# Performance work log

Measured on AMD Instinct MI355X. Metric: run time of the kernel, lower is better.

## Reference

```python
import jax, jax.numpy as jnp
import numpy as np

K = 32
BN_EPS = 1e-5


def setup_inputs() -> dict:
    key = jax.random.key(0)
    ks = jax.random.split(key, 4)
    B, Cin, N, C = 8, 1152, 4096, 128
    return {
        "x": jax.random.normal(ks[0], (B, Cin, N), dtype=jnp.float32),
        "W1": jax.random.normal(ks[1], (C, Cin), dtype=jnp.float32) * 0.02,
        "bn_gamma": jnp.ones((C,), jnp.float32),
        "bn_beta": jnp.zeros((C,), jnp.float32),
        "bn_mean": jnp.zeros((C,), jnp.float32),
        "bn_var": jnp.ones((C,), jnp.float32),
        "Wq": jax.random.normal(ks[2], (C, C), dtype=jnp.float32) * 0.05,
        "Wk": jax.random.normal(ks[3], (C, C), dtype=jnp.float32) * 0.05,
    }


def _forward(x, W1, bn_gamma, bn_beta, bn_mean, bn_var, Wq, Wk):
    # conv1: 1x1 Conv1d (no bias) + BatchNorm (inference stats) + LeakyReLU(0.2)
    h = jnp.einsum('oc,bcn->bon', W1, x)                       # [B,128,N]
    h = (h - bn_mean[None, :, None]) * jax.lax.rsqrt(bn_var + BN_EPS)[None, :, None]
    h = h * bn_gamma[None, :, None] + bn_beta[None, :, None]
    h = jnp.where(h >= 0, h, 0.2 * h)
    f = jnp.transpose(h, (0, 2, 1))                            # [B,N,128]

    # ops.group: feature-space KNN + 'diff' grouping
    sq = jnp.sum(f * f, axis=-1)                               # [B,N]
    dist = sq[:, :, None] + sq[:, None, :] - 2.0 * jnp.einsum('bnc,bmc->bnm', f, f)
    _, idx = jax.lax.top_k(-dist, K)                           # [B,N,K]
    nb = jax.vmap(lambda fb, ib: fb[ib])(f, idx)               # [B,N,K,128]
    diff = nb - f[:, :, None, :]                               # neighbors - center

    # q/k 1x1 convs, per-point 1xK attention
    q = jnp.einsum('bnc,oc->bno', f, Wq)                       # [B,N,128]
    k = jnp.einsum('bnkc,oc->bnko', diff, Wk)                  # [B,N,K,128]
    energy = jnp.einsum('bnc,bnkc->bnk', q, k) / jnp.sqrt(jnp.float32(q.shape[-1]))
    attn = jax.nn.softmax(energy, axis=-1)                     # [B,N,K]

    # std over K (biased), then per-cloud standardize (unbiased std, torch default)
    s = jnp.std(attn, axis=-1)                                 # [B,N]
    mean = jnp.mean(s, axis=1, keepdims=True)
    std = jnp.std(s, axis=1, keepdims=True, ddof=1)
    z = (s - mean) / std
    return 1.0 / (1.0 + jnp.power(jnp.float32(20.0), -z))      # modified sigmoid


def reference(x, W1, bn_gamma, bn_beta, bn_mean, bn_var, Wq, Wk):
    return _forward(x, W1, bn_gamma, bn_beta, bn_mean, bn_var, Wq, Wk)
```

## Files before the change

### kernel.cpp

```cpp
#include <hip/hip_runtime.h>
#include <math.h>

#define B_   8
#define CIN  1152
#define NPTS 4096
#define CH   128
#define KNN  32

__global__ __launch_bounds__(256) void k_conv_bn(
    const float* __restrict__ x, const float* __restrict__ W1,
    const float* __restrict__ gamma, const float* __restrict__ beta,
    const float* __restrict__ bmean, const float* __restrict__ bvar,
    float* __restrict__ f)
{
  __shared__ float Wl[8][132];
  __shared__ float Xl[8][64];
  int bid = blockIdx.x;
  int b = bid & 7;
  int nbase = (bid >> 3) * 64;
  int t = threadIdx.x;
  int c0 = (t & 31) * 4, n0 = (t >> 5) * 8;
  double acc[4][8];
#pragma unroll
  for (int i = 0; i < 4; ++i)
#pragma unroll
    for (int j = 0; j < 8; ++j) acc[i][j] = 0.0;

  for (int k0 = 0; k0 < CIN; k0 += 8) {
    {
      int c = t >> 1, kp = (t & 1) * 4;
      float4 w4 = *(const float4*)&W1[(size_t)c * CIN + k0 + kp];
      Wl[kp + 0][c] = w4.x; Wl[kp + 1][c] = w4.y;
      Wl[kp + 2][c] = w4.z; Wl[kp + 3][c] = w4.w;
    }
    {
      int k = t >> 5, n = (t & 31) * 2;
      float2 x2 = *(const float2*)&x[((size_t)b * CIN + (k0 + k)) * NPTS + nbase + n];
      Xl[k][n] = x2.x; Xl[k][n + 1] = x2.y;
    }
    __syncthreads();
#pragma unroll
    for (int kk = 0; kk < 8; ++kk) {
      float4 a  = *(const float4*)&Wl[kk][c0];
      float4 b0 = *(const float4*)&Xl[kk][n0];
      float4 b1 = *(const float4*)&Xl[kk][n0 + 4];
      double av[4] = {(double)a.x, (double)a.y, (double)a.z, (double)a.w};
      double bv[8] = {(double)b0.x, (double)b0.y, (double)b0.z, (double)b0.w,
                      (double)b1.x, (double)b1.y, (double)b1.z, (double)b1.w};
#pragma unroll
      for (int i = 0; i < 4; ++i)
#pragma unroll
        for (int j = 0; j < 8; ++j) acc[i][j] = fma(av[i], bv[j], acc[i][j]);
    }
    __syncthreads();
  }
  double rs[4], gm[4], bt[4], mu[4];
#pragma unroll
  for (int i = 0; i < 4; ++i) {
    int c = c0 + i;
    rs[i] = 1.0 / sqrt((double)bvar[c] + 1e-5);
    gm[i] = (double)gamma[c]; bt[i] = (double)beta[c]; mu[i] = (double)bmean[c];
  }
#pragma unroll
  for (int j = 0; j < 8; ++j) {
    int n = nbase + n0 + j;
    float4 o;
    float* op = &o.x;
#pragma unroll
    for (int i = 0; i < 4; ++i) {
      double v = (acc[i][j] - mu[i]) * rs[i];
      v = v * gm[i] + bt[i];
      if (v < 0.0) v = 0.2 * v;
      op[i] = (float)v;
    }
    *(float4*)&f[((size_t)b * NPTS + n) * CH + c0] = o;
  }
}

__global__ __launch_bounds__(256) void k_sq(const float* __restrict__ f,
                                            double* __restrict__ sq)
{
  int row = blockIdx.x * 4 + (threadIdx.x >> 6);
  int lane = threadIdx.x & 63;
  float2 v = ((const float2*)f)[(size_t)row * 64 + lane];
  double s = (double)v.x * (double)v.x + (double)v.y * (double)v.y;
#pragma unroll
  for (int sft = 1; sft < 64; sft <<= 1) s += __shfl_xor(s, sft);
  if (lane == 0) sq[row] = s;
}

__global__ __launch_bounds__(256) void k_wqk(const float* __restrict__ Wq,
                                             const float* __restrict__ Wk,
                                             float* __restrict__ M)
{
  __shared__ float Ql[128][17];
  __shared__ float Kl[128][17];
  int t = threadIdx.x;
  int cb = blockIdx.x * 16;
  int db = blockIdx.y * 16;
  {
    int o = t >> 1, h = (t & 1) * 8;
    float4 a = *(const float4*)&Wq[(size_t)o * CH + cb + h];
    float4 b = *(const float4*)&Wq[(size_t)o * CH + cb + h + 4];
    Ql[o][h + 0] = a.x; Ql[o][h + 1] = a.y; Ql[o][h + 2] = a.z; Ql[o][h + 3] = a.w;
    Ql[o][h + 4] = b.x; Ql[o][h + 5] = b.y; Ql[o][h + 6] = b.z; Ql[o][h + 7] = b.w;
    float4 c4 = *(const float4*)&Wk[(size_t)o * CH + db + h];
    float4 d4 = *(const float4*)&Wk[(size_t)o * CH + db + h + 4];
    Kl[o][h + 0] = c4.x; Kl[o][h + 1] = c4.y; Kl[o][h + 2] = c4.z; Kl[o][h + 3] = c4.w;
    Kl[o][h + 4] = d4.x; Kl[o][h + 5] = d4.y; Kl[o][h + 6] = d4.z; Kl[o][h + 7] = d4.w;
  }
  __syncthreads();
  int ci = t >> 4, cj = t & 15;
  float acc = 0.f;
#pragma unroll 8
  for (int o = 0; o < 128; ++o) acc = fmaf(Ql[o][ci], Kl[o][cj], acc);
  M[(size_t)(cb + ci) * CH + db + cj] = acc;
}

__global__ __launch_bounds__(256) void k_qk(const float* __restrict__ f,
                                            const float* __restrict__ M,
                                            float* __restrict__ qk)
{
  __shared__ float Ft[128][68];
  __shared__ float Ml[128 * 128];
  int t = threadIdx.x;
  size_t rbase = (size_t)blockIdx.x * 64;
  {
    int r = t & 63, cp = (t >> 6) * 32;
    for (int i = 0; i < 8; ++i) {
      int c = cp + i * 4;
      float4 v = *(const float4*)&f[(rbase + r) * CH + c];
      Ft[c][r] = v.x; Ft[c + 1][r] = v.y; Ft[c + 2][r] = v.z; Ft[c + 3][r] = v.w;
    }
  }
  {
    const float4* Mg = (const float4*)M;
    float4* Md = (float4*)Ml;
    for (int i = 0; i < 16; ++i) Md[t + 256 * i] = Mg[t + 256 * i];
  }
  __syncthreads();
  int r0 = (t >> 4) * 4, c0 = (t & 15) * 8;
  float acc[4][8];
#pragma unroll
  for (int i = 0; i < 4; ++i)
#pragma unroll
    for (int j = 0; j < 8; ++j) acc[i][j] = 0.f;
#pragma unroll 8
  for (int k = 0; k < 128; ++k) {
    float4 a  = *(const float4*)&Ft[k][r0];
    float4 b0 = *(const float4*)&Ml[k * 128 + c0];
    float4 b1 = *(const float4*)&Ml[k * 128 + c0 + 4];
    float av[4] = {a.x, a.y, a.z, a.w};
    float bv[8] = {b0.x, b0.y, b0.z, b0.w, b1.x, b1.y, b1.z, b1.w};
#pragma unroll
    for (int i = 0; i < 4; ++i)
#pragma unroll
      for (int j = 0; j < 8; ++j) acc[i][j] = fmaf(av[i], bv[j], acc[i][j]);
  }
#pragma unroll
  for (int i = 0; i < 4; ++i) {
    float4 o0 = {acc[i][0], acc[i][1], acc[i][2], acc[i][3]};
    float4 o1 = {acc[i][4], acc[i][5], acc[i][6], acc[i][7]};
    *(float4*)&qk[(rbase + r0 + i) * CH + c0]     = o0;
    *(float4*)&qk[(rbase + r0 + i) * CH + c0 + 4] = o1;
  }
}

__global__ __launch_bounds__(256) void k_dist(
    const float* __restrict__ f, const double* __restrict__ sq,
    float* __restrict__ D, int b, int rowoff)
{
  __shared__ float As[128][68];
  __shared__ float Bs[128][68];
  int t = threadIdx.x;
  int nb = rowoff + blockIdx.x * 64;
  int mb = blockIdx.y * 64;
  const float* fb = f + (size_t)b * NPTS * CH;
  {
    int r = t & 63, cq = (t >> 6) * 32;
    for (int i = 0; i < 8; ++i) {
      int c = cq + i * 4;
      float4 v = *(const float4*)&fb[(size_t)(nb + r) * CH + c];
      As[c][r] = v.x; As[c + 1][r] = v.y; As[c + 2][r] = v.z; As[c + 3][r] = v.w;
      float4 u = *(const float4*)&fb[(size_t)(mb + r) * CH + c];
      Bs[c][r] = u.x; Bs[c + 1][r] = u.y; Bs[c + 2][r] = u.z; Bs[c + 3][r] = u.w;
    }
  }
  __syncthreads();
  int r0 = (t >> 4) * 4, m0 = (t & 15) * 4;
  double acc[4][4];
#pragma unroll
  for (int i = 0; i < 4; ++i)
#pragma unroll
    for (int j = 0; j < 4; ++j) acc[i][j] = 0.0;
#pragma unroll 4
  for (int c = 0; c < 128; ++c) {
    float4 a  = *(const float4*)&As[c][r0];
    float4 bb = *(const float4*)&Bs[c][m0];
    double av[4] = {(double)a.x, (double)a.y, (double)a.z, (double)a.w};
    double bv[4] = {(double)bb.x, (double)bb.y, (double)bb.z, (double)bb.w};
#pragma unroll
    for (int i = 0; i < 4; ++i)
#pragma unroll
      for (int j = 0; j < 4; ++j) acc[i][j] = fma(av[i], bv[j], acc[i][j]);
  }
  double sqm[4];
#pragma unroll
  for (int j = 0; j < 4; ++j) sqm[j] = sq[(size_t)b * NPTS + mb + m0 + j];
#pragma unroll
  for (int i = 0; i < 4; ++i) {
    double sqn = sq[(size_t)b * NPTS + nb + r0 + i];
    float4 o;
    o.x = (float)((sqn + sqm[0]) - 2.0 * acc[i][0]);
    o.y = (float)((sqn + sqm[1]) - 2.0 * acc[i][1]);
    o.z = (float)((sqn + sqm[2]) - 2.0 * acc[i][2]);
    o.w = (float)((sqn + sqm[3]) - 2.0 * acc[i][3]);
    int rloc = blockIdx.x * 64 + r0 + i;
    *(float4*)&D[(size_t)rloc * NPTS + mb + m0] = o;
  }
}

__device__ __forceinline__ unsigned int sortkey(float x) {
  unsigned int u = __float_as_uint(x);
  return (u & 0x80000000u) ? ~u : (u | 0x80000000u);
}

__global__ __launch_bounds__(256) void k_select(
    const float* __restrict__ D, const float* __restrict__ f,
    const float* __restrict__ qk, float* __restrict__ sv,
    int b, int rowoff)
{
  __shared__ unsigned int keys[NPTS];
  __shared__ unsigned int hist[256];
  __shared__ unsigned int wsum[4];
  __shared__ unsigned int eqw[4];
  __shared__ unsigned int sh_bucket, sh_excl, nkept;
  __shared__ int   kept[KNN];
  __shared__ float qkl[CH];
  __shared__ float fc[CH];
  __shared__ float eng[KNN];

  int t = threadIdx.x;
  int row = rowoff + blockIdx.x;
  const float* fb = f + (size_t)b * NPTS * CH;

  {
    const float4* Dp = (const float4*)(D + (size_t)blockIdx.x * NPTS);
#pragma unroll
    for (int i = 0; i < 4; ++i) {
      float4 v = Dp[t + 256 * i];
      uint4 u;
      u.x = sortkey(v.x); u.y = sortkey(v.y);
      u.z = sortkey(v.z); u.w = sortkey(v.w);
      ((uint4*)keys)[t + 256 * i] = u;
    }
  }
  if (t == 0) nkept = 0;
  if (t < 32) {
    ((float4*)qkl)[t] = ((const float4*)(qk + ((size_t)b * NPTS + row) * CH))[t];
  } else if (t < 64) {
    ((float4*)fc)[t - 32] = ((const float4*)(fb + (size_t)row * CH))[t - 32];
  }
  __syncthreads();

  unsigned int prefix = 0;
  unsigned int target = KNN;
  unsigned int cnt_less = 0;
  for (int pass = 0; pass < 4; ++pass) {
    int shift = 24 - pass * 8;
    hist[t] = 0;
    __syncthreads();
#pragma unroll
    for (int i = 0; i < 16; ++i) {
      unsigned int k = keys[t + 256 * i];
      bool m = (pass == 0) || ((k >> (shift + 8)) == prefix);
      if (m) atomicAdd(&hist[(k >> shift) & 255u], 1u);
    }
    __syncthreads();
    unsigned int v = hist[t];
    unsigned int sc = v;
#pragma unroll
    for (int d = 1; d < 64; d <<= 1) {
      unsigned int nn = __shfl_up(sc, d);
      if ((t & 63) >= d) sc += nn;
    }
    if ((t & 63) == 63) wsum[t >> 6] = sc;
    __syncthreads();
    unsigned int wo = 0;
#pragma unroll
    for (int w = 0; w < 4; ++w) wo += (w < (t >> 6)) ? wsum[w] : 0u;
    unsigned int incl = sc + wo;
    unsigned int excl = incl - v;
    if (excl < target && target <= incl) { sh_bucket = (unsigned int)t; sh_excl = excl; }
    __syncthreads();
    prefix = (prefix << 8) | sh_bucket;
    target -= sh_excl;
    cnt_less += sh_excl;
    __syncthreads();
  }
  unsigned int thr_key = prefix;

#pragma unroll
  for (int i = 0; i < 16; ++i) {
    int idx = t + 256 * i;
    if (keys[idx] < thr_key) {
      unsigned int p = atomicAdd(&nkept, 1u);
      kept[p] = idx;
    }
  }
  {
    unsigned int eqloc = 0;
#pragma unroll
    for (int j = 0; j < 16; ++j) eqloc += (keys[t * 16 + j] == thr_key) ? 1u : 0u;
    unsigned int esc = eqloc;
#pragma unroll
    for (int d = 1; d < 64; d <<= 1) {
      unsigned int nn = __shfl_up(esc, d);
      if ((t & 63) >= d) esc += nn;
    }
    if ((t & 63) == 63) eqw[t >> 6] = esc;
    __syncthreads();
    unsigned int ewo = 0;
#pragma unroll
    for (int w = 0; w < 4; ++w) ewo += (w < (t >> 6)) ? eqw[w] : 0u;
    unsigned int slot = cnt_less + (esc + ewo - eqloc);
#pragma unroll
    for (int j = 0; j < 16; ++j) {
      if (keys[t * 16 + j] == thr_key) {
        if (slot < KNN) kept[slot] = t * 16 + j;
        slot++;
      }
    }
  }
  __syncthreads();

  {
    int kk = t >> 3, lg = t & 7;
    int mg = kept[kk];
    const float* fm = fb + (size_t)mg * CH;
    float dd = 0.f, ds = 0.f;
#pragma unroll
    for (int i = 0; i < 4; ++i) {
      float4 qv = *(const float4*)&qkl[lg * 16 + i * 4];
      float4 vm = *(const float4*)&fm[lg * 16 + i * 4];
      float4 vc = *(const float4*)&fc[lg * 16 + i * 4];
      dd = fmaf(qv.x, vm.x, dd); dd = fmaf(qv.y, vm.y, dd);
      dd = fmaf(qv.z, vm.z, dd); dd = fmaf(qv.w, vm.w, dd);
      ds = fmaf(qv.x, vc.x, ds); ds = fmaf(qv.y, vc.y, ds);
      ds = fmaf(qv.z, vc.z, ds); ds = fmaf(qv.w, vc.w, ds);
    }
#pragma unroll
    for (int m = 1; m < 8; m <<= 1) { dd += __shfl_xor(dd, m); ds += __shfl_xor(ds, m); }
    if (lg == 0) eng[kk] = (dd - ds) * 0.08838834764831845f;
  }
  __syncthreads();

  if (t < 64) {
    float e = (t < 32) ? eng[t] : -INFINITY;
    float mx = e;
#pragma unroll
    for (int m = 1; m < 32; m <<= 1) mx = fmaxf(mx, __shfl_xor(mx, m));
    float ex = (t < 32) ? expf(e - mx) : 0.f;
    float sm = ex;
#pragma unroll
    for (int m = 1; m < 32; m <<= 1) sm += __shfl_xor(sm, m);
    float a  = (t < 32) ? (ex / sm) : 0.f;
    float sa = a;
#pragma unroll
    for (int m = 1; m < 32; m <<= 1) sa += __shfl_xor(sa, m);
    float mean = sa * (1.f / 32.f);
    float dv = (t < 32) ? (a - mean) : 0.f;
    float vr = dv * dv;
#pragma unroll
    for (int m = 1; m < 32; m <<= 1) vr += __shfl_xor(vr, m);
    if (t == 0) sv[(size_t)b * NPTS + row] = sqrtf(vr * (1.f / 32.f));
  }
}

__global__ __launch_bounds__(256) void k_final(const float* __restrict__ s,
                                               float* __restrict__ out)
{
  __shared__ float red[4];
  int b = blockIdx.x, t = threadIdx.x;
  const float4* sp = (const float4*)(s + (size_t)b * NPTS);
  float4* op = (float4*)(out + (size_t)b * NPTS);
  float4 vs[4];
  float loc = 0.f;
#pragma unroll
  for (int i = 0; i < 4; ++i) {
    vs[i] = sp[t + 256 * i];
    loc += vs[i].x + vs[i].y + vs[i].z + vs[i].w;
  }
#pragma unroll
  for (int sft = 1; sft < 64; sft <<= 1) loc += __shfl_xor(loc, sft);
  if ((t & 63) == 0) red[t >> 6] = loc;
  __syncthreads();
  float meanv = (red[0] + red[1] + red[2] + red[3]) * (1.f / 4096.f);
  __syncthreads();
  float loc2 = 0.f;
#pragma unroll
  for (int i = 0; i < 4; ++i) {
    float dx = vs[i].x - meanv, dy = vs[i].y - meanv;
    float dz = vs[i].z - meanv, dw = vs[i].w - meanv;
    loc2 += dx * dx + dy * dy + dz * dz + dw * dw;
  }
#pragma unroll
  for (int sft = 1; sft < 64; sft <<= 1) loc2 += __shfl_xor(loc2, sft);
  if ((t & 63) == 0) red[t >> 6] = loc2;
  __syncthreads();
  float var = (red[0] + red[1] + red[2] + red[3]) * (1.f / 4095.f);
  float rstd = rsqrtf(var);
  const float L20 = 4.3219280948873623f;
#pragma unroll
  for (int i = 0; i < 4; ++i) {
    float4 v = vs[i], o;
    o.x = 1.f / (1.f + exp2f(-(v.x - meanv) * rstd * L20));
    o.y = 1.f / (1.f + exp2f(-(v.y - meanv) * rstd * L20));
    o.z = 1.f / (1.f + exp2f(-(v.z - meanv) * rstd * L20));
    o.w = 1.f / (1.f + exp2f(-(v.w - meanv) * rstd * L20));
    op[t + 256 * i] = o;
  }
}

extern "C" void kernel_launch(void* const* d_in, const int* in_sizes, int n_in,
                              void* d_out, int out_size, void* d_ws, size_t ws_size,
                              hipStream_t stream)
{
  const float* x     = (const float*)d_in[0];
  const float* W1    = (const float*)d_in[1];
  const float* gamma = (const float*)d_in[2];
  const float* beta  = (const float*)d_in[3];
  const float* bmean = (const float*)d_in[4];
  const float* bvar  = (const float*)d_in[5];
  const float* Wq    = (const float*)d_in[6];
  const float* Wk    = (const float*)d_in[7];
  float* out = (float*)d_out;

  float*  f   = (float*)d_ws;
  float*  qk  = f  + (size_t)B_ * NPTS * CH;
  double* sqd = (double*)(qk + (size_t)B_ * NPTS * CH);
  float*  sv  = (float*)(sqd + (size_t)B_ * NPTS);
  float*  M   = sv + (size_t)B_ * NPTS;
  float*  D   = M  + (size_t)CH * CH;

  size_t fixed_bytes = (size_t)((char*)D - (char*)d_ws);
  size_t avail = (ws_size > fixed_bytes) ? (ws_size - fixed_bytes) : 0;
  int chunk = 1024;
  if (avail >= (size_t)4096 * NPTS * 4) chunk = 4096;
  else if (avail >= (size_t)2048 * NPTS * 4) chunk = 2048;

  hipLaunchKernelGGL(k_conv_bn, dim3(512), dim3(256), 0, stream,
                     x, W1, gamma, beta, bmean, bvar, f);
  hipLaunchKernelGGL(k_sq, dim3(8192), dim3(256), 0, stream, f, sqd);
  hipLaunchKernelGGL(k_wqk, dim3(8, 8), dim3(256), 0, stream, Wq, Wk, M);
  hipLaunchKernelGGL(k_qk, dim3(512), dim3(256), 0, stream, f, M, qk);
  for (int b = 0; b < B_; ++b) {
    for (int ro = 0; ro < NPTS; ro += chunk) {
      hipLaunchKernelGGL(k_dist, dim3(chunk / 64, 64), dim3(256), 0, stream,
                         f, sqd, D, b, ro);
      hipLaunchKernelGGL(k_select, dim3(chunk), dim3(256), 0, stream,
                         D, f, qk, sv, b, ro);
    }
  }
  hipLaunchKernelGGL(k_final, dim3(8), dim3(256), 0, stream, sv, out);
}
```

Baseline: 2.165 ms.

## Enlarge distance tile to 128x128 with register prefetch; privatize select histograms

The distance kernel now computes a 128x128 output tile per block, 8x8 per thread, in fp64, and prefetches the next LDS row into registers. This raises arithmetic intensity per LDS load. The select kernel gives each wavefront its own histogram copy to cut atomic contention, and rotates the equality-count scan to avoid LDS bank conflicts. The risks are heavy register pressure from 64 double accumulators and LDS use of about 132KB per dist block, which may not fit or may limit occupancy.

```diff
diff --git a/kernel.cpp b/kernel.cpp
--- a/kernel.cpp
+++ b/kernel.cpp
@@ -170,15 +170,16 @@
     const float* __restrict__ f, const double* __restrict__ sq,
     float* __restrict__ D, int b, int rowoff)
 {
-  __shared__ float As[128][68];
-  __shared__ float Bs[128][68];
+  __shared__ float As[128][132];
+  __shared__ float Bs[128][132];
   int t = threadIdx.x;
-  int nb = rowoff + blockIdx.x * 64;
-  int mb = blockIdx.y * 64;
+  int nb = rowoff + blockIdx.x * 128;
+  int mb = blockIdx.y * 128;
   const float* fb = f + (size_t)b * NPTS * CH;
   {
-    int r = t & 63, cq = (t >> 6) * 32;
-    for (int i = 0; i < 8; ++i) {
+    int r = t & 127, cq = (t >> 7) * 64;
+#pragma unroll
+    for (int i = 0; i < 16; ++i) {
       int c = cq + i * 4;
       float4 v = *(const float4*)&fb[(size_t)(nb + r) * CH + c];
       As[c][r] = v.x; As[c + 1][r] = v.y; As[c + 2][r] = v.z; As[c + 3][r] = v.w;
@@ -187,36 +188,54 @@
     }
   }
   __syncthreads();
-  int r0 = (t >> 4) * 4, m0 = (t & 15) * 4;
-  double acc[4][4];
-#pragma unroll
-  for (int i = 0; i < 4; ++i)
-#pragma unroll
-    for (int j = 0; j < 4; ++j) acc[i][j] = 0.0;
-#pragma unroll 4
+  int r0 = (t >> 4) * 8, m0 = (t & 15) * 8;
+  double acc[8][8];
+#pragma unroll
+  for (int i = 0; i < 8; ++i)
+#pragma unroll
+    for (int j = 0; j < 8; ++j) acc[i][j] = 0.0;
+
+  float4 a0 = *(const float4*)&As[0][r0];
+  float4 a1 = *(const float4*)&As[0][r0 + 4];
+  float4 b0 = *(const float4*)&Bs[0][m0];
+  float4 b1 = *(const float4*)&Bs[0][m0 + 4];
+#pragma unroll 2
   for (int c = 0; c < 128; ++c) {
-    float4 a  = *(const float4*)&As[c][r0];
-    float4 bb = *(const float4*)&Bs[c][m0];
-    double av[4] = {(double)a.x, (double)a.y, (double)a.z, (double)a.w};
-    double bv[4] = {(double)bb.x, (double)bb.y, (double)bb.z, (double)bb.w};
-#pragma unroll
-    for (int i = 0; i < 4; ++i)
-#pragma unroll
-      for (int j = 0; j < 4; ++j) acc[i][j] = fma(av[i], bv[j], acc[i][j]);
-  }
-  double sqm[4];
-#pragma unroll
-  for (int j = 0; j < 4; ++j) sqm[j] = sq[(size_t)b * NPTS + mb + m0 + j];
-#pragma unroll
-  for (int i = 0; i < 4; ++i) {
-    double sqn = sq[(size_t)b * NPTS + nb + r0 + i];
+    int cn = (c + 1) & 127;
+    float4 na0 = *(const float4*)&As[cn][r0];
+    float4 na1 = *(const float4*)&As[cn][r0 + 4];
+    float4 nb0 = *(const float4*)&Bs[cn][m0];
+    float4 nb1 = *(const float4*)&Bs[cn][m0 + 4];
+    double av[8] = {(double)a0.x, (double)a0.y, (double)a0.z, (double)a0.w,
+                    (double)a1.x, (double)a1.y, (double)a1.z, (double)a1.w};
+    double bv[8] = {(double)b0.x, (double)b0.y, (double)b0.z, (double)b0.w,
+                    (double)b1.x, (double)b1.y, (double)b1.z, (double)b1.w};
+#pragma unroll
+    for (int i = 0; i < 8; ++i)
+#pragma unroll
+      for (int j = 0; j < 8; ++j) acc[i][j] = fma(av[i], bv[j], acc[i][j]);
+    a0 = na0; a1 = na1; b0 = nb0; b1 = nb1;
+  }
+
+  double sqn[8], sqm[8];
+#pragma unroll
+  for (int i = 0; i < 8; ++i) sqn[i] = sq[(size_t)b * NPTS + nb + r0 + i];
+#pragma unroll
+  for (int j = 0; j < 8; ++j) sqm[j] = sq[(size_t)b * NPTS + mb + m0 + j];
+#pragma unroll
+  for (int i = 0; i < 8; ++i) {
+    int rloc = blockIdx.x * 128 + r0 + i;
     float4 o;
-    o.x = (float)((sqn + sqm[0]) - 2.0 * acc[i][0]);
-    o.y = (float)((sqn + sqm[1]) - 2.0 * acc[i][1]);
-    o.z = (float)((sqn + sqm[2]) - 2.0 * acc[i][2]);
-    o.w = (float)((sqn + sqm[3]) - 2.0 * acc[i][3]);
-    int rloc = blockIdx.x * 64 + r0 + i;
+    o.x = (float)((sqn[i] + sqm[0]) - 2.0 * acc[i][0]);
+    o.y = (float)((sqn[i] + sqm[1]) - 2.0 * acc[i][1]);
+    o.z = (float)((sqn[i] + sqm[2]) - 2.0 * acc[i][2]);
+    o.w = (float)((sqn[i] + sqm[3]) - 2.0 * acc[i][3]);
     *(float4*)&D[(size_t)rloc * NPTS + mb + m0] = o;
+    o.x = (float)((sqn[i] + sqm[4]) - 2.0 * acc[i][4]);
+    o.y = (float)((sqn[i] + sqm[5]) - 2.0 * acc[i][5]);
+    o.z = (float)((sqn[i] + sqm[6]) - 2.0 * acc[i][6]);
+    o.w = (float)((sqn[i] + sqm[7]) - 2.0 * acc[i][7]);
+    *(float4*)&D[(size_t)rloc * NPTS + mb + m0 + 4] = o;
   }
 }
 
@@ -231,7 +250,7 @@
     int b, int rowoff)
 {
   __shared__ unsigned int keys[NPTS];
-  __shared__ unsigned int hist[256];
+  __shared__ unsigned int hist[4][257];
   __shared__ unsigned int wsum[4];
   __shared__ unsigned int eqw[4];
   __shared__ unsigned int sh_bucket, sh_excl, nkept;
@@ -266,18 +285,19 @@
   unsigned int prefix = 0;
   unsigned int target = KNN;
   unsigned int cnt_less = 0;
+  int wv = t >> 6;
   for (int pass = 0; pass < 4; ++pass) {
     int shift = 24 - pass * 8;
-    hist[t] = 0;
+    hist[0][t] = 0; hist[1][t] = 0; hist[2][t] = 0; hist[3][t] = 0;
     __syncthreads();
 #pragma unroll
     for (int i = 0; i < 16; ++i) {
       unsigned int k = keys[t + 256 * i];
       bool m = (pass == 0) || ((k >> (shift + 8)) == prefix);
-      if (m) atomicAdd(&hist[(k >> shift) & 255u], 1u);
-    }
-    __syncthreads();
-    unsigned int v = hist[t];
+      if (m) atomicAdd(&hist[wv][(k >> shift) & 255u], 1u);
+    }
+    __syncthreads();
+    unsigned int v = hist[0][t] + hist[1][t] + hist[2][t] + hist[3][t];
     unsigned int sc = v;
 #pragma unroll
     for (int d = 1; d < 64; d <<= 1) {
@@ -311,7 +331,8 @@
   {
     unsigned int eqloc = 0;
 #pragma unroll
-    for (int j = 0; j < 16; ++j) eqloc += (keys[t * 16 + j] == thr_key) ? 1u : 0u;
+    for (int j = 0; j < 16; ++j)
+      eqloc += (keys[t * 16 + ((j + t) & 15)] == thr_key) ? 1u : 0u;
     unsigned int esc = eqloc;
 #pragma unroll
     for (int d = 1; d < 64; d <<= 1) {
@@ -456,7 +477,7 @@
   hipLaunchKernelGGL(k_qk, dim3(512), dim3(256), 0, stream, f, M, qk);
   for (int b = 0; b < B_; ++b) {
     for (int ro = 0; ro < NPTS; ro += chunk) {
-      hipLaunchKernelGGL(k_dist, dim3(chunk / 64, 64), dim3(256), 0, stream,
+      hipLaunchKernelGGL(k_dist, dim3(chunk / 128, 32), dim3(256), 0, stream,
                          f, sqd, D, b, ro);
       hipLaunchKernelGGL(k_select, dim3(chunk), dim3(256), 0, stream,
                          D, f, qk, sv, b, ro);
```

Measured after the change: 2.333 ms. 1.08x slower.
